# Performance work log

Hardware: AMD Instinct MI355X
Metric: run time of the kernel (lower is better)

The kernel has to match this reference:

```python
import jax, jax.numpy as jnp
import numpy as np

N_HEADS, D_MODEL, D_HEAD = 16, 1024, 64
BATCH, SEQ = 2, 2048
INIT_RANGE = 0.02


def setup_inputs() -> dict:
    key = jax.random.key(0)
    ks = jax.random.split(key, 5)
    x = jax.random.normal(ks[0], (BATCH, SEQ, D_MODEL), dtype=jnp.float32)
    W_Q = jax.random.normal(ks[1], (N_HEADS, D_MODEL, D_HEAD), dtype=jnp.float32) * INIT_RANGE
    W_K = jax.random.normal(ks[2], (N_HEADS, D_MODEL, D_HEAD), dtype=jnp.float32) * INIT_RANGE
    W_V = jax.random.normal(ks[3], (N_HEADS, D_MODEL, D_HEAD), dtype=jnp.float32) * INIT_RANGE
    W_O = jax.random.normal(ks[4], (N_HEADS, D_HEAD, D_MODEL), dtype=jnp.float32) * INIT_RANGE
    b_Q = jnp.zeros((N_HEADS, D_HEAD), dtype=jnp.float32)
    b_K = jnp.zeros((N_HEADS, D_HEAD), dtype=jnp.float32)
    b_V = jnp.zeros((N_HEADS, D_HEAD), dtype=jnp.float32)
    b_O = jnp.zeros((D_MODEL,), dtype=jnp.float32)
    return {"normalized_resid_pre": x, "W_Q": W_Q, "W_K": W_K, "W_V": W_V,
            "W_O": W_O, "b_Q": b_Q, "b_K": b_K, "b_V": b_V, "b_O": b_O}


def reference(normalized_resid_pre, W_Q, W_K, W_V, W_O, b_Q, b_K, b_V, b_O):
    x = normalized_resid_pre  # [b, s, d_model]
    q = jnp.einsum('bsm,hmd->bshd', x, W_Q) + b_Q  # [b, s, h, d_head]
    k = jnp.einsum('bsm,hmd->bshd', x, W_K) + b_K
    v = jnp.einsum('bsm,hmd->bshd', x, W_V) + b_V
    scores = jnp.einsum('bqhd,bkhd->bhqk', q, k) / jnp.sqrt(jnp.float32(D_HEAD))
    seq = x.shape[1]
    causal = jnp.tril(jnp.ones((seq, seq), dtype=bool))  # True where allowed
    scores = jnp.where(causal, scores, jnp.float32(-jnp.inf))
    pattern = jax.nn.softmax(scores, axis=-1)  # [b, h, q, k]
    z = jnp.einsum('bhqk,bkhd->bqhd', pattern, v)
    attn_out = jnp.einsum('bqhd,hdm->bqm', z, W_O) + b_O
    return attn_out
```

## Files before the change

kernel.cpp:

```cpp
#include <hip/hip_runtime.h>
#include <hip/hip_bf16.h>

#define BATCH 2
#define SEQL 2048
#define NH 16
#define DH 64
#define DM 1024
#define LDK 72
#define QSCALE 0.1803368801111244f

typedef __hip_bfloat16 bf16;
typedef __attribute__((ext_vector_type(8))) short  bf16x8;
typedef __attribute__((ext_vector_type(4))) float  f32x4;

__device__ __forceinline__ void gl_lds16(const void* g, void* l) {
    __builtin_amdgcn_global_load_lds(
        (const __attribute__((address_space(1))) unsigned int*)g,
        (__attribute__((address_space(3))) unsigned int*)l, 16, 0, 0);
}

__global__ __launch_bounds__(256) void prep_kernel(
    const float* __restrict__ x,
    const float* __restrict__ Wq, const float* __restrict__ Wk,
    const float* __restrict__ Wv, const float* __restrict__ Wo,
    bf16* __restrict__ Wt, bf16* __restrict__ xb)
{
    const int zi = blockIdx.z;
    if (zi == 4) {
        const int bid = blockIdx.y * 16 + blockIdx.x;
        const size_t base = ((size_t)bid * 256 + threadIdx.x) * 4;
        #pragma unroll
        for (int it = 0; it < 16; ++it) {
            const size_t i = base + (size_t)it * 262144;
            const float4 v = *(const float4*)(x + i);
            bf16 o[4];
            o[0] = __float2bfloat16(v.x); o[1] = __float2bfloat16(v.y);
            o[2] = __float2bfloat16(v.z); o[3] = __float2bfloat16(v.w);
            *(uint2*)(xb + i) = *(const uint2*)o;
        }
        return;
    }

    __shared__ float ts[64][65];
    const float* src = (zi == 0) ? Wq : (zi == 1) ? Wk : (zi == 2) ? Wv : Wo;
    bf16* dst = Wt + (size_t)zi * DM * DM;
    const int row0 = blockIdx.y * 64;
    const int col0 = blockIdx.x * 64;
    const int tx = threadIdx.x & 63;
    const int ty = threadIdx.x >> 6;

    if (zi < 3) {
        const int h = col0 >> 6;
        #pragma unroll
        for (int i = 0; i < 16; ++i) {
            const int r = ty + 4 * i;
            ts[r][tx] = src[h * (DM * DH) + (row0 + r) * DH + tx];
        }
    } else {
        #pragma unroll
        for (int i = 0; i < 16; ++i) {
            const int r = ty + 4 * i;
            ts[r][tx] = src[(size_t)(row0 + r) * DM + col0 + tx];
        }
    }
    __syncthreads();
    #pragma unroll
    for (int i = 0; i < 16; ++i) {
        const int rr = ty + 4 * i;
        dst[(size_t)(col0 + rr) * DM + row0 + tx] = __float2bfloat16(ts[tx][rr]);
    }
}

__global__ __launch_bounds__(256) void qkv_gemm(
    const bf16* __restrict__ xb, const bf16* __restrict__ Wt,
    const float* __restrict__ bq, const float* __restrict__ bk, const float* __restrict__ bv,
    bf16* __restrict__ qkv)
{
    __shared__ __align__(16) bf16 As[2][128 * 32];
    __shared__ __align__(16) bf16 Bs[2][128 * 32];

    const int t = threadIdx.x;
    const int lane = t & 63, w = t >> 6;
    const int ml = lane & 15, quad = lane >> 4;
    const int wr = w >> 1, wc = w & 1;
    const int bn = blockIdx.x, bm = blockIdx.y, which = blockIdx.z;

    const bf16* A0 = xb + (size_t)(bm * 128) * DM;
    const bf16* B0 = Wt + (size_t)which * DM * DM + (size_t)(bn * 128) * DM;
    const float* bias = (which == 0) ? bq : (which == 1) ? bk : bv;
    bf16* outb = qkv + (size_t)which * (BATCH * SEQL * NH * DH);
    const float oscale = (which == 0) ? QSCALE : 1.0f;

    f32x4 acc[4][4];
    #pragma unroll
    for (int i = 0; i < 4; ++i)
        #pragma unroll
        for (int j = 0; j < 4; ++j) acc[i][j] = (f32x4){0.f, 0.f, 0.f, 0.f};

    const int r0 = t >> 2, c0 = (t & 3) * 8;
    const int f1 = t + 256;
    const int r1 = f1 >> 2, c1 = (f1 & 3) * 8;

    for (int kt = 0; kt < DM / 64; ++kt) {
        const int k0 = kt * 64;
        __syncthreads();
        #pragma unroll
        for (int half = 0; half < 2; ++half) {
            const int kh = k0 + half * 32;
            gl_lds16(A0 + (size_t)r0 * DM + kh + c0, &As[half][t * 8]);
            gl_lds16(A0 + (size_t)r1 * DM + kh + c1, &As[half][f1 * 8]);
            gl_lds16(B0 + (size_t)r0 * DM + kh + c0, &Bs[half][t * 8]);
            gl_lds16(B0 + (size_t)r1 * DM + kh + c1, &Bs[half][f1 * 8]);
        }
        __syncthreads();
        #pragma unroll
        for (int half = 0; half < 2; ++half) {
            bf16x8 af[4], bfr[4];
            #pragma unroll
            for (int i = 0; i < 4; ++i)
                af[i] = *(const bf16x8*)&As[half][(wr * 64 + i * 16 + ml) * 32 + quad * 8];
            #pragma unroll
            for (int j = 0; j < 4; ++j)
                bfr[j] = *(const bf16x8*)&Bs[half][(wc * 64 + j * 16 + ml) * 32 + quad * 8];
            #pragma unroll
            for (int i = 0; i < 4; ++i)
                #pragma unroll
                for (int j = 0; j < 4; ++j)
                    acc[i][j] = __builtin_amdgcn_mfma_f32_16x16x32_bf16(af[i], bfr[j], acc[i][j], 0, 0, 0);
        }
    }

    float bb[4];
    #pragma unroll
    for (int j = 0; j < 4; ++j) bb[j] = bias[bn * 128 + wc * 64 + j * 16 + ml];

    if (which == 2) {
        #pragma unroll
        for (int i = 0; i < 4; ++i) {
            const int row0v = bm * 128 + wr * 64 + i * 16 + quad * 4;
            const int b = row0v >> 11;
            const int s0 = row0v & (SEQL - 1);
            #pragma unroll
            for (int j = 0; j < 4; ++j) {
                const int col = bn * 128 + wc * 64 + j * 16 + ml;
                const int h = col >> 6, d = col & 63;
                bf16 tmp[4];
                #pragma unroll
                for (int rg = 0; rg < 4; ++rg)
                    tmp[rg] = __float2bfloat16(acc[i][j][rg] + bb[j]);
                *(uint2*)&outb[(((size_t)(b * NH + h)) * DH + d) * SEQL + s0] =
                    *(const uint2*)tmp;
            }
        }
    } else {
        #pragma unroll
        for (int i = 0; i < 4; ++i) {
            #pragma unroll
            for (int rg = 0; rg < 4; ++rg) {
                const int row = bm * 128 + wr * 64 + i * 16 + quad * 4 + rg;
                const int b = row >> 11;
                const int s = row & (SEQL - 1);
                #pragma unroll
                for (int j = 0; j < 4; ++j) {
                    const int col = bn * 128 + wc * 64 + j * 16 + ml;
                    const int h = col >> 6, d = col & 63;
                    outb[(((size_t)(b * NH + h)) * SEQL + s) * DH + d] =
                        __float2bfloat16((acc[i][j][rg] + bb[j]) * oscale);
                }
            }
        }
    }
}

__global__ __launch_bounds__(256) void oproj_gemm(
    const bf16* __restrict__ zb, const bf16* __restrict__ Bt,
    const float* __restrict__ bo, float* __restrict__ out)
{
    __shared__ __align__(16) bf16 As[2][128 * 32];
    __shared__ __align__(16) bf16 Bs[2][64 * 32];

    const int t = threadIdx.x;
    const int lane = t & 63, w = t >> 6;
    const int ml = lane & 15, quad = lane >> 4;
    const int wr = w >> 1, wc = w & 1;
    const int bn = blockIdx.x, bm = blockIdx.y;

    const bf16* A0 = zb + (size_t)(bm * 128) * DM;
    const bf16* B0 = Bt + (size_t)(bn * 64) * DM;

    f32x4 acc[4][2];
    #pragma unroll
    for (int i = 0; i < 4; ++i)
        #pragma unroll
        for (int j = 0; j < 2; ++j) acc[i][j] = (f32x4){0.f, 0.f, 0.f, 0.f};

    const int r0 = t >> 2, c0 = (t & 3) * 8;
    const int f1 = t + 256;
    const int r1 = f1 >> 2, c1 = (f1 & 3) * 8;

    for (int kt = 0; kt < DM / 64; ++kt) {
        const int k0 = kt * 64;
        __syncthreads();
        #pragma unroll
        for (int half = 0; half < 2; ++half) {
            const int kh = k0 + half * 32;
            gl_lds16(A0 + (size_t)r0 * DM + kh + c0, &As[half][t * 8]);
            gl_lds16(A0 + (size_t)r1 * DM + kh + c1, &As[half][f1 * 8]);
            gl_lds16(B0 + (size_t)r0 * DM + kh + c0, &Bs[half][t * 8]);
        }
        __syncthreads();
        #pragma unroll
        for (int half = 0; half < 2; ++half) {
            bf16x8 af[4], bfr[2];
            #pragma unroll
            for (int i = 0; i < 4; ++i)
                af[i] = *(const bf16x8*)&As[half][(wr * 64 + i * 16 + ml) * 32 + quad * 8];
            #pragma unroll
            for (int j = 0; j < 2; ++j)
                bfr[j] = *(const bf16x8*)&Bs[half][(wc * 32 + j * 16 + ml) * 32 + quad * 8];
            #pragma unroll
            for (int i = 0; i < 4; ++i)
                #pragma unroll
                for (int j = 0; j < 2; ++j)
                    acc[i][j] = __builtin_amdgcn_mfma_f32_16x16x32_bf16(af[i], bfr[j], acc[i][j], 0, 0, 0);
        }
    }

    float bb[2];
    #pragma unroll
    for (int j = 0; j < 2; ++j) bb[j] = bo[bn * 64 + wc * 32 + j * 16 + ml];

    #pragma unroll
    for (int i = 0; i < 4; ++i) {
        #pragma unroll
        for (int rg = 0; rg < 4; ++rg) {
            const int row = bm * 128 + wr * 64 + i * 16 + quad * 4 + rg;
            #pragma unroll
            for (int j = 0; j < 2; ++j) {
                const int col = bn * 64 + wc * 32 + j * 16 + ml;
                out[(size_t)row * DM + col] = acc[i][j][rg] + bb[j];
            }
        }
    }
}

__global__ __launch_bounds__(256) void attn_kernel(
    const bf16* __restrict__ qg, const bf16* __restrict__ kg, const bf16* __restrict__ vtg,
    bf16* __restrict__ z)
{
    __shared__ __align__(16) bf16 KsS[64 * 64];
    __shared__ __align__(16) bf16 VtS[64 * 64];
    __shared__ bf16 PsS[4][16 * LDK];

    const int t    = threadIdx.x;
    const int lane = t & 63;
    const int w    = t >> 6;
    const int m    = lane & 15;
    const int quad = lane >> 4;

    const int bh = blockIdx.x;
    const int b  = bh >> 4;
    const int h  = bh & 15;
    const int qt = (gridDim.y - 1) - blockIdx.y;
    const int q0 = qt * 64;

    const size_t base   = (size_t)bh * SEQL * DH;
    const size_t vtbase = (size_t)bh * DH * SEQL;

    const int s0 = w * 128 + lane;
    const int s1 = s0 + 64;
    const int r0s = s0 >> 3, c0s = (s0 & 7) ^ (r0s & 7);
    const int r1s = s1 >> 3, c1s = (s1 & 7) ^ (r1s & 7);

    bf16x8 aq[2];
    {
        const bf16* qp = qg + base + (size_t)(q0 + w * 16 + m) * DH + quad * 8;
        aq[0] = *(const bf16x8*)(qp);
        aq[1] = *(const bf16x8*)(qp + 32);
    }

    const short ob = (m == 0) ? (short)0x3F80 : (short)0;
    const bf16x8 bones = {ob, ob, ob, ob, ob, ob, ob, ob};

    f32x4 zacc[4];
    #pragma unroll
    for (int nt = 0; nt < 4; ++nt) zacc[nt] = (f32x4){0.f, 0.f, 0.f, 0.f};
    f32x4 lacc = (f32x4){0.f, 0.f, 0.f, 0.f};

    bf16* Psw = PsS[w];

    for (int kt = 0; kt <= qt; ++kt) {
        __syncthreads();
        {
            const int kc = kt * 64;
            gl_lds16(kg + base + (size_t)(kc + r0s) * DH + c0s * 8, &KsS[s0 * 8]);
            gl_lds16(kg + base + (size_t)(kc + r1s) * DH + c1s * 8, &KsS[s1 * 8]);
            gl_lds16(vtg + vtbase + (size_t)r0s * SEQL + kc + c0s * 8, &VtS[s0 * 8]);
            gl_lds16(vtg + vtbase + (size_t)r1s * SEQL + kc + c1s * 8, &VtS[s1 * 8]);
        }
        __syncthreads();

        f32x4 sc[4];
        #pragma unroll
        for (int nt = 0; nt < 4; ++nt) sc[nt] = (f32x4){0.f, 0.f, 0.f, 0.f};
        #pragma unroll
        for (int ks = 0; ks < 2; ++ks) {
            #pragma unroll
            for (int nt = 0; nt < 4; ++nt) {
                const int row = nt * 16 + m;
                const int pc  = ((ks << 2) + quad) ^ (m & 7);
                const bf16x8 bk = *(const bf16x8*)(&KsS[row * 64 + pc * 8]);
                sc[nt] = __builtin_amdgcn_mfma_f32_16x16x32_bf16(aq[ks], bk, sc[nt], 0, 0, 0);
            }
        }
        if (kt == qt) {
            #pragma unroll
            for (int nt = 0; nt < 4; ++nt) {
                const int col = nt * 16 + m;
                #pragma unroll
                for (int rg = 0; rg < 4; ++rg) {
                    const int row = w * 16 + quad * 4 + rg;
                    if (col > row) sc[nt][rg] = -1e30f;
                }
            }
        }

        #pragma unroll
        for (int nt = 0; nt < 4; ++nt)
            #pragma unroll
            for (int rg = 0; rg < 4; ++rg)
                Psw[(quad * 4 + rg) * LDK + nt * 16 + m] =
                    __float2bfloat16(__builtin_exp2f(sc[nt][rg]));

        #pragma unroll
        for (int ks = 0; ks < 2; ++ks) {
            const bf16x8 ap = *(const bf16x8*)(&Psw[m * LDK + ks * 32 + quad * 8]);
            lacc = __builtin_amdgcn_mfma_f32_16x16x32_bf16(ap, bones, lacc, 0, 0, 0);
            #pragma unroll
            for (int nt = 0; nt < 4; ++nt) {
                const int row = nt * 16 + m;
                const int pc  = ((ks << 2) + quad) ^ (m & 7);
                const bf16x8 bv = *(const bf16x8*)(&VtS[row * 64 + pc * 8]);
                zacc[nt] = __builtin_amdgcn_mfma_f32_16x16x32_bf16(ap, bv, zacc[nt], 0, 0, 0);
            }
        }
    }

    float invl[4];
    #pragma unroll
    for (int rg = 0; rg < 4; ++rg)
        invl[rg] = 1.f / __shfl(lacc[rg], quad * 16);
    #pragma unroll
    for (int nt = 0; nt < 4; ++nt) {
        const int d = nt * 16 + m;
        #pragma unroll
        for (int rg = 0; rg < 4; ++rg) {
            const int qrow = q0 + w * 16 + quad * 4 + rg;
            z[(((size_t)b * SEQL + qrow) * NH + h) * DH + d] =
                __float2bfloat16(zacc[nt][rg] * invl[rg]);
        }
    }
}

extern "C" void kernel_launch(void* const* d_in, const int* in_sizes, int n_in,
                              void* d_out, int out_size, void* d_ws, size_t ws_size,
                              hipStream_t stream)
{
    const float* x  = (const float*)d_in[0];
    const float* Wq = (const float*)d_in[1];
    const float* Wk = (const float*)d_in[2];
    const float* Wv = (const float*)d_in[3];
    const float* Wo = (const float*)d_in[4];
    const float* bq = (const float*)d_in[5];
    const float* bk = (const float*)d_in[6];
    const float* bv = (const float*)d_in[7];
    const float* bo = (const float*)d_in[8];
    float* out = (float*)d_out;

    const size_t TOK = (size_t)BATCH * SEQL;
    const size_t QKV = TOK * DM;
    bf16* xb  = (bf16*)d_ws;
    bf16* Wt  = xb + QKV;
    bf16* qkv = Wt + 4 * (size_t)DM * DM;
    bf16* zb  = qkv + 3 * QKV;

    prep_kernel<<<dim3(16, 16, 5), 256, 0, stream>>>(x, Wq, Wk, Wv, Wo, Wt, xb);
    qkv_gemm<<<dim3(8, 32, 3), 256, 0, stream>>>(xb, Wt, bq, bk, bv, qkv);
    attn_kernel<<<dim3(BATCH * NH, SEQL / 64), 256, 0, stream>>>(
        qkv, qkv + QKV, qkv + 2 * QKV, zb);
    oproj_gemm<<<dim3(16, 32), 256, 0, stream>>>(zb, Wt + 3 * (size_t)DM * DM, bo, out);
}
```

Before: 188.2 us.

## Double-buffer K/V tiles in LDS and raise wave priority around MFMA

The attention kernel now keeps two LDS buffers each for K and V^T. It preloads the first tile, then at each iteration issues async global-to-LDS loads for the next tile before computing on the current one. This overlaps memory latency with the QK^T and PV MFMA work and drops one of the two barriers per iteration. It also wraps the MFMA phases in s_setprio to favour matrix issue. The cost is double the K/V LDS footprint, which may reduce occupancy, and correctness now depends on the compiler waiting on the async LDS loads before the barrier.

```diff
diff --git a/kernel.cpp b/kernel.cpp
--- a/kernel.cpp
+++ b/kernel.cpp
@@ -248,8 +248,8 @@
     const bf16* __restrict__ qg, const bf16* __restrict__ kg, const bf16* __restrict__ vtg,
     bf16* __restrict__ z)
 {
-    __shared__ __align__(16) bf16 KsS[64 * 64];
-    __shared__ __align__(16) bf16 VtS[64 * 64];
+    __shared__ __align__(16) bf16 KsS[2][64 * 64];
+    __shared__ __align__(16) bf16 VtS[2][64 * 64];
     __shared__ bf16 PsS[4][16 * LDK];
 
     const int t    = threadIdx.x;
@@ -289,30 +289,45 @@
 
     bf16* Psw = PsS[w];
 
+    {
+        gl_lds16(kg + base + (size_t)r0s * DH + c0s * 8, &KsS[0][s0 * 8]);
+        gl_lds16(kg + base + (size_t)r1s * DH + c1s * 8, &KsS[0][s1 * 8]);
+        gl_lds16(vtg + vtbase + (size_t)r0s * SEQL + c0s * 8, &VtS[0][s0 * 8]);
+        gl_lds16(vtg + vtbase + (size_t)r1s * SEQL + c1s * 8, &VtS[0][s1 * 8]);
+    }
+
     for (int kt = 0; kt <= qt; ++kt) {
+        const int cur = kt & 1;
         __syncthreads();
-        {
-            const int kc = kt * 64;
-            gl_lds16(kg + base + (size_t)(kc + r0s) * DH + c0s * 8, &KsS[s0 * 8]);
-            gl_lds16(kg + base + (size_t)(kc + r1s) * DH + c1s * 8, &KsS[s1 * 8]);
-            gl_lds16(vtg + vtbase + (size_t)r0s * SEQL + kc + c0s * 8, &VtS[s0 * 8]);
-            gl_lds16(vtg + vtbase + (size_t)r1s * SEQL + kc + c1s * 8, &VtS[s1 * 8]);
-        }
-        __syncthreads();
+
+        if (kt < qt) {
+            const int kc = (kt + 1) * 64;
+            bf16* Kd = &KsS[cur ^ 1][0];
+            bf16* Vd = &VtS[cur ^ 1][0];
+            gl_lds16(kg + base + (size_t)(kc + r0s) * DH + c0s * 8, Kd + s0 * 8);
+            gl_lds16(kg + base + (size_t)(kc + r1s) * DH + c1s * 8, Kd + s1 * 8);
+            gl_lds16(vtg + vtbase + (size_t)r0s * SEQL + kc + c0s * 8, Vd + s0 * 8);
+            gl_lds16(vtg + vtbase + (size_t)r1s * SEQL + kc + c1s * 8, Vd + s1 * 8);
+        }
+
+        const bf16* Ks = &KsS[cur][0];
+        const bf16* Vt = &VtS[cur][0];
 
         f32x4 sc[4];
         #pragma unroll
         for (int nt = 0; nt < 4; ++nt) sc[nt] = (f32x4){0.f, 0.f, 0.f, 0.f};
+        __builtin_amdgcn_s_setprio(1);
         #pragma unroll
         for (int ks = 0; ks < 2; ++ks) {
             #pragma unroll
             for (int nt = 0; nt < 4; ++nt) {
                 const int row = nt * 16 + m;
                 const int pc  = ((ks << 2) + quad) ^ (m & 7);
-                const bf16x8 bk = *(const bf16x8*)(&KsS[row * 64 + pc * 8]);
+                const bf16x8 bk = *(const bf16x8*)(&Ks[row * 64 + pc * 8]);
                 sc[nt] = __builtin_amdgcn_mfma_f32_16x16x32_bf16(aq[ks], bk, sc[nt], 0, 0, 0);
             }
         }
+        __builtin_amdgcn_s_setprio(0);
         if (kt == qt) {
             #pragma unroll
             for (int nt = 0; nt < 4; ++nt) {
@@ -332,6 +347,7 @@
                 Psw[(quad * 4 + rg) * LDK + nt * 16 + m] =
                     __float2bfloat16(__builtin_exp2f(sc[nt][rg]));
 
+        __builtin_amdgcn_s_setprio(1);
         #pragma unroll
         for (int ks = 0; ks < 2; ++ks) {
             const bf16x8 ap = *(const bf16x8*)(&Psw[m * LDK + ks * 32 + quad * 8]);
@@ -340,10 +356,11 @@
             for (int nt = 0; nt < 4; ++nt) {
                 const int row = nt * 16 + m;
                 const int pc  = ((ks << 2) + quad) ^ (m & 7);
-                const bf16x8 bv = *(const bf16x8*)(&VtS[row * 64 + pc * 8]);
+                const bf16x8 bv = *(const bf16x8*)(&Vt[row * 64 + pc * 8]);
                 zacc[nt] = __builtin_amdgcn_mfma_f32_16x16x32_bf16(ap, bv, zacc[nt], 0, 0, 0);
             }
         }
+        __builtin_amdgcn_s_setprio(0);
     }
 
     float invl[4];
```

Measured after the change: 185.1 us. No clear change (-1.7%).

## Pair causal query tiles per block with split-K wave groups for balance

Applied to the files above, without the earlier changes.

Each 512-thread block now handles two query tiles, qa and 31-qa, so every block does the same amount of causal work. It shares K/V tile loads across both tiles. For key tiles past qa, the two wave halves split the 64 keys and their partial accumulators are reduced through LDS at the end. It also adds s_setprio around the MFMA sections. In exchange the block is larger, there is an extra LDS reduction phase, and more control flow inside the loop.

```diff
diff --git a/kernel.cpp b/kernel.cpp
--- a/kernel.cpp
+++ b/kernel.cpp
@@ -244,39 +244,45 @@
     }
 }
 
-__global__ __launch_bounds__(256) void attn_kernel(
+__global__ __launch_bounds__(512) void attn_kernel(
     const bf16* __restrict__ qg, const bf16* __restrict__ kg, const bf16* __restrict__ vtg,
     bf16* __restrict__ z)
 {
     __shared__ __align__(16) bf16 KsS[64 * 64];
     __shared__ __align__(16) bf16 VtS[64 * 64];
-    __shared__ bf16 PsS[4][16 * LDK];
+    __shared__ __align__(16) bf16 PsS[8][16 * LDK];
 
     const int t    = threadIdx.x;
     const int lane = t & 63;
     const int w    = t >> 6;
     const int m    = lane & 15;
     const int quad = lane >> 4;
+    const int wg   = w & 3;
+    const int half = w >> 2;
 
     const int bh = blockIdx.x;
     const int b  = bh >> 4;
     const int h  = bh & 15;
-    const int qt = (gridDim.y - 1) - blockIdx.y;
-    const int q0 = qt * 64;
+    const int qa = blockIdx.y;
+    const int qb = 31 - qa;
+    const int q0a = qa * 64;
+    const int q0b = qb * 64;
 
     const size_t base   = (size_t)bh * SEQL * DH;
     const size_t vtbase = (size_t)bh * DH * SEQL;
 
-    const int s0 = w * 128 + lane;
-    const int s1 = s0 + 64;
-    const int r0s = s0 >> 3, c0s = (s0 & 7) ^ (r0s & 7);
-    const int r1s = s1 >> 3, c1s = (s1 & 7) ^ (r1s & 7);
-
-    bf16x8 aq[2];
+    const int s  = t;
+    const int rs = s >> 3, cs = (s & 7) ^ (rs & 7);
+
+    bf16x8 aq[2], aqB[2];
     {
-        const bf16* qp = qg + base + (size_t)(q0 + w * 16 + m) * DH + quad * 8;
+        const int myq = (w < 4) ? (q0a + w * 16) : (q0b + wg * 16);
+        const bf16* qp = qg + base + (size_t)(myq + m) * DH + quad * 8;
         aq[0] = *(const bf16x8*)(qp);
         aq[1] = *(const bf16x8*)(qp + 32);
+        const bf16* qpb = qg + base + (size_t)(q0b + wg * 16 + m) * DH + quad * 8;
+        aqB[0] = *(const bf16x8*)(qpb);
+        aqB[1] = *(const bf16x8*)(qpb + 32);
     }
 
     const short ob = (m == 0) ? (short)0x3F80 : (short)0;
@@ -289,75 +295,176 @@
 
     bf16* Psw = PsS[w];
 
-    for (int kt = 0; kt <= qt; ++kt) {
+    for (int kt = 0; kt <= qb; ++kt) {
         __syncthreads();
         {
             const int kc = kt * 64;
-            gl_lds16(kg + base + (size_t)(kc + r0s) * DH + c0s * 8, &KsS[s0 * 8]);
-            gl_lds16(kg + base + (size_t)(kc + r1s) * DH + c1s * 8, &KsS[s1 * 8]);
-            gl_lds16(vtg + vtbase + (size_t)r0s * SEQL + kc + c0s * 8, &VtS[s0 * 8]);
-            gl_lds16(vtg + vtbase + (size_t)r1s * SEQL + kc + c1s * 8, &VtS[s1 * 8]);
-        }
-        __syncthreads();
-
-        f32x4 sc[4];
-        #pragma unroll
-        for (int nt = 0; nt < 4; ++nt) sc[nt] = (f32x4){0.f, 0.f, 0.f, 0.f};
-        #pragma unroll
-        for (int ks = 0; ks < 2; ++ks) {
-            #pragma unroll
-            for (int nt = 0; nt < 4; ++nt) {
-                const int row = nt * 16 + m;
-                const int pc  = ((ks << 2) + quad) ^ (m & 7);
-                const bf16x8 bk = *(const bf16x8*)(&KsS[row * 64 + pc * 8]);
-                sc[nt] = __builtin_amdgcn_mfma_f32_16x16x32_bf16(aq[ks], bk, sc[nt], 0, 0, 0);
-            }
-        }
-        if (kt == qt) {
-            #pragma unroll
-            for (int nt = 0; nt < 4; ++nt) {
-                const int col = nt * 16 + m;
-                #pragma unroll
-                for (int rg = 0; rg < 4; ++rg) {
-                    const int row = w * 16 + quad * 4 + rg;
-                    if (col > row) sc[nt][rg] = -1e30f;
-                }
-            }
-        }
-
+            gl_lds16(kg + base + (size_t)(kc + rs) * DH + cs * 8, &KsS[s * 8]);
+            gl_lds16(vtg + vtbase + (size_t)rs * SEQL + kc + cs * 8, &VtS[s * 8]);
+        }
+        __syncthreads();
+
+        if (kt <= qa) {
+            f32x4 sc[4];
+            #pragma unroll
+            for (int nt = 0; nt < 4; ++nt) sc[nt] = (f32x4){0.f, 0.f, 0.f, 0.f};
+            __builtin_amdgcn_s_setprio(1);
+            #pragma unroll
+            for (int ks = 0; ks < 2; ++ks) {
+                #pragma unroll
+                for (int nt = 0; nt < 4; ++nt) {
+                    const int row = nt * 16 + m;
+                    const int pc  = ((ks << 2) + quad) ^ (m & 7);
+                    const bf16x8 bk = *(const bf16x8*)(&KsS[row * 64 + pc * 8]);
+                    sc[nt] = __builtin_amdgcn_mfma_f32_16x16x32_bf16(aq[ks], bk, sc[nt], 0, 0, 0);
+                }
+            }
+            __builtin_amdgcn_s_setprio(0);
+            if (kt == qa && w < 4) {
+                #pragma unroll
+                for (int nt = 0; nt < 4; ++nt) {
+                    const int col = nt * 16 + m;
+                    #pragma unroll
+                    for (int rg = 0; rg < 4; ++rg) {
+                        const int row = wg * 16 + quad * 4 + rg;
+                        if (col > row) sc[nt][rg] = -1e30f;
+                    }
+                }
+            }
+
+            #pragma unroll
+            for (int nt = 0; nt < 4; ++nt)
+                #pragma unroll
+                for (int rg = 0; rg < 4; ++rg)
+                    Psw[(quad * 4 + rg) * LDK + nt * 16 + m] =
+                        __float2bfloat16(__builtin_exp2f(sc[nt][rg]));
+
+            __builtin_amdgcn_s_setprio(1);
+            #pragma unroll
+            for (int ks = 0; ks < 2; ++ks) {
+                const bf16x8 ap = *(const bf16x8*)(&Psw[m * LDK + ks * 32 + quad * 8]);
+                lacc = __builtin_amdgcn_mfma_f32_16x16x32_bf16(ap, bones, lacc, 0, 0, 0);
+                #pragma unroll
+                for (int nt = 0; nt < 4; ++nt) {
+                    const int row = nt * 16 + m;
+                    const int pc  = ((ks << 2) + quad) ^ (m & 7);
+                    const bf16x8 bv = *(const bf16x8*)(&VtS[row * 64 + pc * 8]);
+                    zacc[nt] = __builtin_amdgcn_mfma_f32_16x16x32_bf16(ap, bv, zacc[nt], 0, 0, 0);
+                }
+            }
+            __builtin_amdgcn_s_setprio(0);
+
+            if (kt == qa && w < 4) {
+                float invl[4];
+                #pragma unroll
+                for (int rg = 0; rg < 4; ++rg)
+                    invl[rg] = 1.f / __shfl(lacc[rg], quad * 16);
+                #pragma unroll
+                for (int nt = 0; nt < 4; ++nt) {
+                    const int d = nt * 16 + m;
+                    #pragma unroll
+                    for (int rg = 0; rg < 4; ++rg) {
+                        const int qrow = q0a + wg * 16 + quad * 4 + rg;
+                        z[(((size_t)b * SEQL + qrow) * NH + h) * DH + d] =
+                            __float2bfloat16(zacc[nt][rg] * invl[rg]);
+                    }
+                }
+                #pragma unroll
+                for (int nt = 0; nt < 4; ++nt) zacc[nt] = (f32x4){0.f, 0.f, 0.f, 0.f};
+                lacc = (f32x4){0.f, 0.f, 0.f, 0.f};
+                aq[0] = aqB[0]; aq[1] = aqB[1];
+            }
+        } else {
+            f32x4 sc[2];
+            sc[0] = (f32x4){0.f, 0.f, 0.f, 0.f};
+            sc[1] = (f32x4){0.f, 0.f, 0.f, 0.f};
+            __builtin_amdgcn_s_setprio(1);
+            #pragma unroll
+            for (int ks = 0; ks < 2; ++ks) {
+                #pragma unroll
+                for (int nt = 0; nt < 2; ++nt) {
+                    const int row = half * 32 + nt * 16 + m;
+                    const int pc  = ((ks << 2) + quad) ^ (m & 7);
+                    const bf16x8 bk = *(const bf16x8*)(&KsS[row * 64 + pc * 8]);
+                    sc[nt] = __builtin_amdgcn_mfma_f32_16x16x32_bf16(aq[ks], bk, sc[nt], 0, 0, 0);
+                }
+            }
+            __builtin_amdgcn_s_setprio(0);
+            if (kt == qb) {
+                #pragma unroll
+                for (int nt = 0; nt < 2; ++nt) {
+                    const int col = half * 32 + nt * 16 + m;
+                    #pragma unroll
+                    for (int rg = 0; rg < 4; ++rg) {
+                        const int row = wg * 16 + quad * 4 + rg;
+                        if (col > row) sc[nt][rg] = -1e30f;
+                    }
+                }
+            }
+
+            #pragma unroll
+            for (int nt = 0; nt < 2; ++nt)
+                #pragma unroll
+                for (int rg = 0; rg < 4; ++rg)
+                    Psw[(quad * 4 + rg) * LDK + nt * 16 + m] =
+                        __float2bfloat16(__builtin_exp2f(sc[nt][rg]));
+
+            __builtin_amdgcn_s_setprio(1);
+            {
+                const bf16x8 ap = *(const bf16x8*)(&Psw[m * LDK + quad * 8]);
+                lacc = __builtin_amdgcn_mfma_f32_16x16x32_bf16(ap, bones, lacc, 0, 0, 0);
+                #pragma unroll
+                for (int nt = 0; nt < 4; ++nt) {
+                    const int row = nt * 16 + m;
+                    const int pc  = ((half << 2) + quad) ^ (m & 7);
+                    const bf16x8 bv = *(const bf16x8*)(&VtS[row * 64 + pc * 8]);
+                    zacc[nt] = __builtin_amdgcn_mfma_f32_16x16x32_bf16(ap, bv, zacc[nt], 0, 0, 0);
+                }
+            }
+            __builtin_amdgcn_s_setprio(0);
+        }
+    }
+
+    __syncthreads();
+    if (w < 4) {
+        float* zs = (w < 2) ? ((float*)KsS) + (size_t)w * 1024
+                            : ((float*)VtS) + (size_t)(w - 2) * 1024;
         #pragma unroll
         for (int nt = 0; nt < 4; ++nt)
             #pragma unroll
             for (int rg = 0; rg < 4; ++rg)
-                Psw[(quad * 4 + rg) * LDK + nt * 16 + m] =
-                    __float2bfloat16(__builtin_exp2f(sc[nt][rg]));
-
-        #pragma unroll
-        for (int ks = 0; ks < 2; ++ks) {
-            const bf16x8 ap = *(const bf16x8*)(&Psw[m * LDK + ks * 32 + quad * 8]);
-            lacc = __builtin_amdgcn_mfma_f32_16x16x32_bf16(ap, bones, lacc, 0, 0, 0);
-            #pragma unroll
-            for (int nt = 0; nt < 4; ++nt) {
-                const int row = nt * 16 + m;
-                const int pc  = ((ks << 2) + quad) ^ (m & 7);
-                const bf16x8 bv = *(const bf16x8*)(&VtS[row * 64 + pc * 8]);
-                zacc[nt] = __builtin_amdgcn_mfma_f32_16x16x32_bf16(ap, bv, zacc[nt], 0, 0, 0);
-            }
-        }
-    }
-
-    float invl[4];
-    #pragma unroll
-    for (int rg = 0; rg < 4; ++rg)
-        invl[rg] = 1.f / __shfl(lacc[rg], quad * 16);
-    #pragma unroll
-    for (int nt = 0; nt < 4; ++nt) {
-        const int d = nt * 16 + m;
-        #pragma unroll
-        for (int rg = 0; rg < 4; ++rg) {
-            const int qrow = q0 + w * 16 + quad * 4 + rg;
-            z[(((size_t)b * SEQL + qrow) * NH + h) * DH + d] =
-                __float2bfloat16(zacc[nt][rg] * invl[rg]);
+                zs[lane * 16 + nt * 4 + rg] = zacc[nt][rg];
+        float* ls = ((float*)PsS) + w * 256;
+        #pragma unroll
+        for (int rg = 0; rg < 4; ++rg) ls[lane * 4 + rg] = lacc[rg];
+    }
+    __syncthreads();
+    if (w >= 4) {
+        const int ww = w - 4;
+        const float* zs = (ww < 2) ? ((const float*)KsS) + (size_t)ww * 1024
+                                   : ((const float*)VtS) + (size_t)(ww - 2) * 1024;
+        const float* ls = ((const float*)PsS) + ww * 256;
+        #pragma unroll
+        for (int nt = 0; nt < 4; ++nt)
+            #pragma unroll
+            for (int rg = 0; rg < 4; ++rg)
+                zacc[nt][rg] += zs[lane * 16 + nt * 4 + rg];
+        #pragma unroll
+        for (int rg = 0; rg < 4; ++rg) lacc[rg] += ls[lane * 4 + rg];
+
+        float invl[4];
+        #pragma unroll
+        for (int rg = 0; rg < 4; ++rg)
+            invl[rg] = 1.f / __shfl(lacc[rg], quad * 16);
+        #pragma unroll
+        for (int nt = 0; nt < 4; ++nt) {
+            const int d = nt * 16 + m;
+            #pragma unroll
+            for (int rg = 0; rg < 4; ++rg) {
+                const int qrow = q0b + wg * 16 + quad * 4 + rg;
+                z[(((size_t)b * SEQL + qrow) * NH + h) * DH + d] =
+                    __float2bfloat16(zacc[nt][rg] * invl[rg]);
+            }
         }
     }
 }
@@ -386,7 +493,7 @@
 
     prep_kernel<<<dim3(16, 16, 5), 256, 0, stream>>>(x, Wq, Wk, Wv, Wo, Wt, xb);
     qkv_gemm<<<dim3(8, 32, 3), 256, 0, stream>>>(xb, Wt, bq, bk, bv, qkv);
-    attn_kernel<<<dim3(BATCH * NH, SEQL / 64), 256, 0, stream>>>(
+    attn_kernel<<<dim3(BATCH * NH, 16), 512, 0, stream>>>(
         qkv, qkv + QKV, qkv + 2 * QKV, zb);
     oproj_gemm<<<dim3(16, 32), 256, 0, stream>>>(zb, Wt + 3 * (size_t)DM * DM, bo, out);
 }
```

Result: no change. 184.8 us (-1.8%).

## Enlarge attention tiles to 128 queries and 128 keys, swizzle GEMM block order

Applied to the files above, without the earlier changes.

The attention kernel now handles 128 query rows per block, two 64-row groups per wave, and loads 128-key K/V chunks into LDS. Each K/V fragment is reused across both query groups, which halves the K/V loads and barriers per unit of work, and the loop raises wave priority around the MFMA sections. Both GEMMs remap block indices so that neighbouring blocks share A/B tiles in cache. In exchange the attention grid has half as many blocks, the causal work is less balanced across blocks, and LDS use and register pressure go up.

```diff
diff --git a/kernel.cpp b/kernel.cpp
--- a/kernel.cpp
+++ b/kernel.cpp
@@ -10,8 +10,8 @@
 #define QSCALE 0.1803368801111244f
 
 typedef __hip_bfloat16 bf16;
-typedef __attribute__((ext_vector_type(8))) short  bf16x8;
-typedef __attribute__((ext_vector_type(4))) float  f32x4;
+typedef __attribute__((ext_vector_type(8)))  short bf16x8;
+typedef __attribute__((ext_vector_type(4)))  float f32x4;
 
 __device__ __forceinline__ void gl_lds16(const void* g, void* l) {
     __builtin_amdgcn_global_load_lds(
@@ -83,7 +83,10 @@
     const int lane = t & 63, w = t >> 6;
     const int ml = lane & 15, quad = lane >> 4;
     const int wr = w >> 1, wc = w & 1;
-    const int bn = blockIdx.x, bm = blockIdx.y, which = blockIdx.z;
+    const int bid0 = blockIdx.y * 8 + blockIdx.x;
+    const int L = (bid0 & 7) * 32 + (bid0 >> 3);
+    const int bn = L & 7, bm = L >> 3;
+    const int which = blockIdx.z;
 
     const bf16* A0 = xb + (size_t)(bm * 128) * DM;
     const bf16* B0 = Wt + (size_t)which * DM * DM + (size_t)(bn * 128) * DM;
@@ -183,7 +186,9 @@
     const int lane = t & 63, w = t >> 6;
     const int ml = lane & 15, quad = lane >> 4;
     const int wr = w >> 1, wc = w & 1;
-    const int bn = blockIdx.x, bm = blockIdx.y;
+    const int bid0 = blockIdx.y * 16 + blockIdx.x;
+    const int L = (bid0 & 7) * 64 + (bid0 >> 3);
+    const int bn = L & 15, bm = L >> 4;
 
     const bf16* A0 = zb + (size_t)(bm * 128) * DM;
     const bf16* B0 = Bt + (size_t)(bn * 64) * DM;
@@ -248,9 +253,9 @@
     const bf16* __restrict__ qg, const bf16* __restrict__ kg, const bf16* __restrict__ vtg,
     bf16* __restrict__ z)
 {
-    __shared__ __align__(16) bf16 KsS[64 * 64];
-    __shared__ __align__(16) bf16 VtS[64 * 64];
-    __shared__ bf16 PsS[4][16 * LDK];
+    __shared__ __align__(16) bf16 KsS[128 * 64];
+    __shared__ __align__(16) bf16 VtS[64 * 128];
+    __shared__ __align__(16) bf16 PsS[4][32 * LDK];
 
     const int t    = threadIdx.x;
     const int lane = t & 63;
@@ -259,105 +264,141 @@
     const int quad = lane >> 4;
 
     const int bh = blockIdx.x;
-    const int b  = bh >> 4;
+    const int b0 = bh >> 4;
     const int h  = bh & 15;
-    const int qt = (gridDim.y - 1) - blockIdx.y;
-    const int q0 = qt * 64;
+    const int p  = 15 - (int)blockIdx.y;
 
     const size_t base   = (size_t)bh * SEQL * DH;
     const size_t vtbase = (size_t)bh * DH * SEQL;
 
-    const int s0 = w * 128 + lane;
-    const int s1 = s0 + 64;
-    const int r0s = s0 >> 3, c0s = (s0 & 7) ^ (r0s & 7);
-    const int r1s = s1 >> 3, c1s = (s1 & 7) ^ (r1s & 7);
-
-    bf16x8 aq[2];
-    {
-        const bf16* qp = qg + base + (size_t)(q0 + w * 16 + m) * DH + quad * 8;
-        aq[0] = *(const bf16x8*)(qp);
-        aq[1] = *(const bf16x8*)(qp + 32);
+    int kr[4], kcol[4], vr[4], vcol[4];
+    #pragma unroll
+    for (int i = 0; i < 4; ++i) {
+        const int s = t + 256 * i;
+        kr[i] = s >> 3;  kcol[i] = (s & 7) ^ (kr[i] & 7);
+        vr[i] = s >> 4;  vcol[i] = (s & 15) ^ (vr[i] & 15);
+    }
+
+    bf16x8 aq[2][2];
+    #pragma unroll
+    for (int g = 0; g < 2; ++g) {
+        const bf16* qp = qg + base +
+            (size_t)(p * 128 + g * 64 + w * 16 + m) * DH + quad * 8;
+        aq[g][0] = *(const bf16x8*)(qp);
+        aq[g][1] = *(const bf16x8*)(qp + 32);
     }
 
     const short ob = (m == 0) ? (short)0x3F80 : (short)0;
     const bf16x8 bones = {ob, ob, ob, ob, ob, ob, ob, ob};
 
-    f32x4 zacc[4];
-    #pragma unroll
-    for (int nt = 0; nt < 4; ++nt) zacc[nt] = (f32x4){0.f, 0.f, 0.f, 0.f};
-    f32x4 lacc = (f32x4){0.f, 0.f, 0.f, 0.f};
+    f32x4 zacc[2][4];
+    f32x4 lacc[2];
+    #pragma unroll
+    for (int g = 0; g < 2; ++g) {
+        #pragma unroll
+        for (int nt = 0; nt < 4; ++nt) zacc[g][nt] = (f32x4){0.f, 0.f, 0.f, 0.f};
+        lacc[g] = (f32x4){0.f, 0.f, 0.f, 0.f};
+    }
 
     bf16* Psw = PsS[w];
 
-    for (int kt = 0; kt <= qt; ++kt) {
+    for (int c = 0; c <= p; ++c) {
         __syncthreads();
         {
-            const int kc = kt * 64;
-            gl_lds16(kg + base + (size_t)(kc + r0s) * DH + c0s * 8, &KsS[s0 * 8]);
-            gl_lds16(kg + base + (size_t)(kc + r1s) * DH + c1s * 8, &KsS[s1 * 8]);
-            gl_lds16(vtg + vtbase + (size_t)r0s * SEQL + kc + c0s * 8, &VtS[s0 * 8]);
-            gl_lds16(vtg + vtbase + (size_t)r1s * SEQL + kc + c1s * 8, &VtS[s1 * 8]);
-        }
-        __syncthreads();
-
-        f32x4 sc[4];
-        #pragma unroll
-        for (int nt = 0; nt < 4; ++nt) sc[nt] = (f32x4){0.f, 0.f, 0.f, 0.f};
-        #pragma unroll
-        for (int ks = 0; ks < 2; ++ks) {
-            #pragma unroll
-            for (int nt = 0; nt < 4; ++nt) {
-                const int row = nt * 16 + m;
-                const int pc  = ((ks << 2) + quad) ^ (m & 7);
-                const bf16x8 bk = *(const bf16x8*)(&KsS[row * 64 + pc * 8]);
-                sc[nt] = __builtin_amdgcn_mfma_f32_16x16x32_bf16(aq[ks], bk, sc[nt], 0, 0, 0);
-            }
-        }
-        if (kt == qt) {
-            #pragma unroll
-            for (int nt = 0; nt < 4; ++nt) {
-                const int col = nt * 16 + m;
-                #pragma unroll
-                for (int rg = 0; rg < 4; ++rg) {
-                    const int row = w * 16 + quad * 4 + rg;
-                    if (col > row) sc[nt][rg] = -1e30f;
+            const int kc = c * 128;
+            #pragma unroll
+            for (int i = 0; i < 4; ++i) {
+                gl_lds16(kg + base + (size_t)(kc + kr[i]) * DH + kcol[i] * 8,
+                         &KsS[(t + 256 * i) * 8]);
+                gl_lds16(vtg + vtbase + (size_t)vr[i] * SEQL + kc + vcol[i] * 8,
+                         &VtS[(t + 256 * i) * 8]);
+            }
+        }
+        __syncthreads();
+
+        #pragma unroll
+        for (int c2 = 0; c2 < 2; ++c2) {
+            const int kt = 2 * c + c2;
+            const int co = c2 * 64;
+
+            f32x4 sc[2][4];
+            #pragma unroll
+            for (int g = 0; g < 2; ++g)
+                #pragma unroll
+                for (int nt = 0; nt < 4; ++nt) sc[g][nt] = (f32x4){0.f, 0.f, 0.f, 0.f};
+            __builtin_amdgcn_s_setprio(1);
+            #pragma unroll
+            for (int ks = 0; ks < 2; ++ks) {
+                #pragma unroll
+                for (int nt = 0; nt < 4; ++nt) {
+                    const int rw = co + nt * 16 + m;
+                    const int pc = ((ks << 2) + quad) ^ (m & 7);
+                    const bf16x8 bk = *(const bf16x8*)(&KsS[rw * 64 + pc * 8]);
+                    sc[0][nt] = __builtin_amdgcn_mfma_f32_16x16x32_bf16(aq[0][ks], bk, sc[0][nt], 0, 0, 0);
+                    sc[1][nt] = __builtin_amdgcn_mfma_f32_16x16x32_bf16(aq[1][ks], bk, sc[1][nt], 0, 0, 0);
                 }
             }
-        }
-
-        #pragma unroll
-        for (int nt = 0; nt < 4; ++nt)
-            #pragma unroll
-            for (int rg = 0; rg < 4; ++rg)
-                Psw[(quad * 4 + rg) * LDK + nt * 16 + m] =
-                    __float2bfloat16(__builtin_exp2f(sc[nt][rg]));
-
-        #pragma unroll
-        for (int ks = 0; ks < 2; ++ks) {
-            const bf16x8 ap = *(const bf16x8*)(&Psw[m * LDK + ks * 32 + quad * 8]);
-            lacc = __builtin_amdgcn_mfma_f32_16x16x32_bf16(ap, bones, lacc, 0, 0, 0);
-            #pragma unroll
-            for (int nt = 0; nt < 4; ++nt) {
-                const int row = nt * 16 + m;
-                const int pc  = ((ks << 2) + quad) ^ (m & 7);
-                const bf16x8 bv = *(const bf16x8*)(&VtS[row * 64 + pc * 8]);
-                zacc[nt] = __builtin_amdgcn_mfma_f32_16x16x32_bf16(ap, bv, zacc[nt], 0, 0, 0);
-            }
-        }
-    }
-
-    float invl[4];
-    #pragma unroll
-    for (int rg = 0; rg < 4; ++rg)
-        invl[rg] = 1.f / __shfl(lacc[rg], quad * 16);
-    #pragma unroll
-    for (int nt = 0; nt < 4; ++nt) {
-        const int d = nt * 16 + m;
-        #pragma unroll
-        for (int rg = 0; rg < 4; ++rg) {
-            const int qrow = q0 + w * 16 + quad * 4 + rg;
-            z[(((size_t)b * SEQL + qrow) * NH + h) * DH + d] =
-                __float2bfloat16(zacc[nt][rg] * invl[rg]);
+            __builtin_amdgcn_s_setprio(0);
+
+            #pragma unroll
+            for (int g = 0; g < 2; ++g) {
+                if (kt >= 2 * p + g) {
+                    #pragma unroll
+                    for (int nt = 0; nt < 4; ++nt) {
+                        const int kv = kt * 64 + nt * 16 + m;
+                        #pragma unroll
+                        for (int rg = 0; rg < 4; ++rg) {
+                            const int qr = p * 128 + g * 64 + w * 16 + quad * 4 + rg;
+                            if (kv > qr) sc[g][nt][rg] = -1e30f;
+                        }
+                    }
+                }
+            }
+
+            #pragma unroll
+            for (int g = 0; g < 2; ++g)
+                #pragma unroll
+                for (int nt = 0; nt < 4; ++nt)
+                    #pragma unroll
+                    for (int rg = 0; rg < 4; ++rg)
+                        Psw[(g * 16 + quad * 4 + rg) * LDK + nt * 16 + m] =
+                            __float2bfloat16(__builtin_exp2f(sc[g][nt][rg]));
+
+            __builtin_amdgcn_s_setprio(1);
+            #pragma unroll
+            for (int ks = 0; ks < 2; ++ks) {
+                const bf16x8 ap0 = *(const bf16x8*)(&Psw[(m) * LDK + ks * 32 + quad * 8]);
+                const bf16x8 ap1 = *(const bf16x8*)(&Psw[(16 + m) * LDK + ks * 32 + quad * 8]);
+                lacc[0] = __builtin_amdgcn_mfma_f32_16x16x32_bf16(ap0, bones, lacc[0], 0, 0, 0);
+                lacc[1] = __builtin_amdgcn_mfma_f32_16x16x32_bf16(ap1, bones, lacc[1], 0, 0, 0);
+                #pragma unroll
+                for (int nt = 0; nt < 4; ++nt) {
+                    const int dr = nt * 16 + m;
+                    const int vc = (c2 * 8 + (ks << 2) + quad) ^ m;
+                    const bf16x8 bv = *(const bf16x8*)(&VtS[dr * 128 + vc * 8]);
+                    zacc[0][nt] = __builtin_amdgcn_mfma_f32_16x16x32_bf16(ap0, bv, zacc[0][nt], 0, 0, 0);
+                    zacc[1][nt] = __builtin_amdgcn_mfma_f32_16x16x32_bf16(ap1, bv, zacc[1][nt], 0, 0, 0);
+                }
+            }
+            __builtin_amdgcn_s_setprio(0);
+        }
+    }
+
+    #pragma unroll
+    for (int g = 0; g < 2; ++g) {
+        float invl[4];
+        #pragma unroll
+        for (int rg = 0; rg < 4; ++rg)
+            invl[rg] = 1.f / __shfl(lacc[g][rg], quad * 16);
+        #pragma unroll
+        for (int nt = 0; nt < 4; ++nt) {
+            const int d = nt * 16 + m;
+            #pragma unroll
+            for (int rg = 0; rg < 4; ++rg) {
+                const int qrow = p * 128 + g * 64 + w * 16 + quad * 4 + rg;
+                z[(((size_t)b0 * SEQL + qrow) * NH + h) * DH + d] =
+                    __float2bfloat16(zacc[g][nt][rg] * invl[rg]);
+            }
         }
     }
 }
@@ -386,7 +427,7 @@
 
     prep_kernel<<<dim3(16, 16, 5), 256, 0, stream>>>(x, Wq, Wk, Wv, Wo, Wt, xb);
     qkv_gemm<<<dim3(8, 32, 3), 256, 0, stream>>>(xb, Wt, bq, bk, bv, qkv);
-    attn_kernel<<<dim3(BATCH * NH, SEQL / 64), 256, 0, stream>>>(
+    attn_kernel<<<dim3(BATCH * NH, 16), 256, 0, stream>>>(
         qkv, qkv + QKV, qkv + 2 * QKV, zb);
     oproj_gemm<<<dim3(16, 32), 256, 0, stream>>>(zb, Wt + 3 * (size_t)DM * DM, bo, out);
 }
```

Measured after the change: 193.7 us. 2.9% more time.
